# Performance work log

Measured on AMD Instinct MI355X. Metric: run time of the kernel, lower is better.

Reference implementation:

```python
import jax, jax.numpy as jnp
import numpy as np

MORA_DIV = 2


def setup_inputs() -> dict:
    key = jax.random.key(0)
    k1, k2, k3, k4 = jax.random.split(key, 4)
    d = 4096
    m = d // MORA_DIV
    x = jax.random.normal(k1, (4, 2048, d), dtype=jnp.float32)
    weight = jax.random.normal(k2, (d, d), dtype=jnp.float32) * 0.02
    mora = jax.random.normal(k3, (m, m), dtype=jnp.float32) * 0.02
    # dora_mag initialized as column L2 norm of the frozen weight (1, d_in)
    dora_mag = jnp.linalg.norm(weight, axis=0, keepdims=True)
    return {"x": x, "weight": weight, "mora": mora, "dora_mag": dora_mag}


def reference(x, weight, mora, dora_mag):
    # Tile the small adapter into full (d_out, d_in): repeat_interleave on both dims
    adapter = jnp.repeat(jnp.repeat(mora, MORA_DIV, axis=0), MORA_DIV, axis=1)
    w = weight + adapter                      # (d_out, d_in)
    col_norm = jnp.linalg.norm(w, axis=0, keepdims=True)  # (1, d_in)
    w = dora_mag * (w / col_norm)             # DoRA magnitude rescale
    return jnp.einsum('bsd,od->bso', x, w)    # F.linear, no bias
```

## Files before the change

### kernel.cpp

```cpp
#include <hip/hip_runtime.h>
#include <stdint.h>

#define M_TOT 8192
#define N_TOT 4096
#define K_TOT 4096
#define BM 256
#define BN 256
#define BK 64
#define NIT (K_TOT / (2 * BK))

typedef short  s16x8 __attribute__((ext_vector_type(8)));
typedef unsigned short u16x8 __attribute__((ext_vector_type(8)));
typedef float  f32x4 __attribute__((ext_vector_type(4)));

__device__ __forceinline__ unsigned short f32_to_bf16(float f) {
  union { float f; unsigned u; } v; v.f = f;
  unsigned r = v.u + 0x7FFFu + ((v.u >> 16) & 1u);
  return (unsigned short)(r >> 16);
}

__device__ __forceinline__ void gload_lds16(void* lds, const void* g) {
  __builtin_amdgcn_global_load_lds(
      (const __attribute__((address_space(1))) unsigned int*)g,
      (__attribute__((address_space(3))) unsigned int*)lds,
      16, 0, 0);
}

__global__ void colnorm_partial_k(const float* __restrict__ weight,
                                  const float* __restrict__ mora,
                                  float* __restrict__ partials) {
  int d = blockIdx.x * 256 + threadIdx.x;
  int o0 = blockIdx.y * 128;
  float s = 0.f;
  #pragma unroll 4
  for (int o = o0; o < o0 + 128; ++o) {
    float w = weight[(size_t)o * K_TOT + d] + mora[(size_t)(o >> 1) * 2048 + (d >> 1)];
    s = fmaf(w, w, s);
  }
  partials[blockIdx.y * K_TOT + d] = s;
}

__global__ void scale_k(const float* __restrict__ partials,
                        const float* __restrict__ dora_mag,
                        float* __restrict__ scale) {
  int d = blockIdx.x * 256 + threadIdx.x;
  float s = 0.f;
  #pragma unroll
  for (int c = 0; c < 32; ++c) s += partials[c * K_TOT + d];
  scale[d] = dora_mag[d] / sqrtf(s);
}

__global__ void pack_w_k(const float* __restrict__ weight,
                         const float* __restrict__ mora,
                         const float* __restrict__ scale,
                         unsigned short* __restrict__ wb) {
  size_t idx = ((size_t)blockIdx.x * 256 + threadIdx.x) * 8;
  int o = (int)(idx >> 12);
  int d = (int)(idx & (K_TOT - 1));
  float4 w0 = *(const float4*)(weight + idx);
  float4 w1 = *(const float4*)(weight + idx + 4);
  float4 mv = *(const float4*)(mora + (size_t)(o >> 1) * 2048 + (d >> 1));
  float4 s0 = *(const float4*)(scale + d);
  float4 s1 = *(const float4*)(scale + d + 4);
  u16x8 r;
  r[0] = f32_to_bf16((w0.x + mv.x) * s0.x);
  r[1] = f32_to_bf16((w0.y + mv.x) * s0.y);
  r[2] = f32_to_bf16((w0.z + mv.y) * s0.z);
  r[3] = f32_to_bf16((w0.w + mv.y) * s0.w);
  r[4] = f32_to_bf16((w1.x + mv.z) * s1.x);
  r[5] = f32_to_bf16((w1.y + mv.z) * s1.y);
  r[6] = f32_to_bf16((w1.z + mv.w) * s1.z);
  r[7] = f32_to_bf16((w1.w + mv.w) * s1.w);
  *(u16x8*)(wb + idx) = r;
}

__global__ void pack_x_k(const float* __restrict__ x, unsigned short* __restrict__ xb) {
  size_t idx = ((size_t)blockIdx.x * 256 + threadIdx.x) * 8;
  float4 v0 = *(const float4*)(x + idx);
  float4 v1 = *(const float4*)(x + idx + 4);
  u16x8 r;
  r[0] = f32_to_bf16(v0.x); r[1] = f32_to_bf16(v0.y);
  r[2] = f32_to_bf16(v0.z); r[3] = f32_to_bf16(v0.w);
  r[4] = f32_to_bf16(v1.x); r[5] = f32_to_bf16(v1.y);
  r[6] = f32_to_bf16(v1.z); r[7] = f32_to_bf16(v1.w);
  *(u16x8*)(xb + idx) = r;
}

__global__ void __launch_bounds__(512, 2) gemm_bf16_k(
    const unsigned short* __restrict__ xb,
    const unsigned short* __restrict__ wb,
    float* __restrict__ out) {
  __shared__ short lds[2][2][2][128 * 64];

  const int tid = threadIdx.x;
  const int l   = tid & 63;
  const int wid = tid >> 6;
  const int wm  = wid >> 2;
  const int wn  = wid & 3;
  const int wnh = wn >> 1;

  const int orig = blockIdx.x;
  const int swz  = (orig & 7) * (512 >> 3) + (orig >> 3);
  const int by = swz >> 4;
  const int bx = swz & 15;

  const unsigned short* ag = xb + (size_t)(by * BM) * K_TOT;
  const unsigned short* bg = wb + (size_t)(bx * BN) * K_TOT;

  const int row0 = tid >> 3;
  const int kb0  = (tid & 7) ^ (row0 & 7);
  const int off0 = row0 * K_TOT + kb0 * 8;
  const int off1 = off0 + 64 * K_TOT;
  const int ldst = (tid & ~63) * 8;

  const int lrow = l & 15;
  const int lq   = l >> 4;
  const int key  = lrow & 7;
  const int ab0  = lrow * 64 + ((lq) ^ key) * 8;
  const int ab1  = lrow * 64 + ((4 + lq) ^ key) * 8;

  s16x8 aA[4][2], bB[4][2];
  f32x4 acc[8][4] = {};

#define STAGE(buf, op, h, t) { \
    short* d = &lds[buf][op][h][0] + ldst; \
    const unsigned short* s = ((op) ? bg : ag) + (size_t)(h) * 128 * K_TOT + (size_t)(t) * BK; \
    gload_lds16(d, s + off0); \
    gload_lds16(d + 4096, s + off1); }
#define DSA(buf, mh) { const short* p = &lds[buf][0][wm][0]; \
    _Pragma("unroll") for (int mm = 0; mm < 4; ++mm) { \
      aA[mm][0] = *(const s16x8*)(p + ((mh) * 4 + mm) * 1024 + ab0); \
      aA[mm][1] = *(const s16x8*)(p + ((mh) * 4 + mm) * 1024 + ab1); } }
#define DSB(buf, nh) { const short* p = &lds[buf][1][wnh][0] + (wn & 1) * 4096; \
    _Pragma("unroll") for (int nn = 0; nn < 2; ++nn) { \
      bB[(nh) * 2 + nn][0] = *(const s16x8*)(p + ((nh) * 2 + nn) * 1024 + ab0); \
      bB[(nh) * 2 + nn][1] = *(const s16x8*)(p + ((nh) * 2 + nn) * 1024 + ab1); } }
#define MMQ(mh, nh) { __builtin_amdgcn_s_setprio(1); \
    _Pragma("unroll") for (int mm = 0; mm < 4; ++mm) \
      _Pragma("unroll") for (int nn = 0; nn < 2; ++nn) \
        _Pragma("unroll") for (int kh = 0; kh < 2; ++kh) \
          acc[(mh) * 4 + mm][(nh) * 2 + nn] = __builtin_amdgcn_mfma_f32_16x16x32_bf16( \
              aA[mm][kh], bB[(nh) * 2 + nn][kh], acc[(mh) * 4 + mm][(nh) * 2 + nn], 0, 0, 0); \
    __builtin_amdgcn_s_setprio(0); }
#define BARm()  asm volatile("s_barrier" ::: "memory")
#define VM6()   asm volatile("s_waitcnt vmcnt(6)" ::: "memory")
#define VM4()   asm volatile("s_waitcnt vmcnt(4)" ::: "memory")
#define VM0()   asm volatile("s_waitcnt vmcnt(0)" ::: "memory")

  STAGE(0, 0, 0, 0); STAGE(0, 0, 1, 0); STAGE(0, 1, 0, 0); STAGE(0, 1, 1, 0);
  STAGE(1, 1, 0, 1); STAGE(1, 1, 1, 1); STAGE(1, 0, 0, 1);
  VM6(); BARm();

  #pragma unroll 1
  for (int i = 0; i < NIT - 1; ++i) {
    const int t1 = 2 * i + 1;
    const int t2 = t1 + 1;
    const int t3 = t1 + 2;
    DSA(0, 0); DSB(0, 0); MMQ(0, 0); DSB(0, 1); STAGE(1, 0, 1, t1); BARm();
    MMQ(0, 1); DSA(0, 1); BARm();
    MMQ(1, 0); STAGE(0, 1, 0, t2); BARm();
    MMQ(1, 1); STAGE(0, 1, 1, t2); VM4(); BARm();
    DSA(1, 0); DSB(1, 0); MMQ(0, 0); DSB(1, 1); STAGE(0, 0, 0, t2); BARm();
    MMQ(0, 1); DSA(1, 1); STAGE(0, 0, 1, t2); BARm();
    MMQ(1, 0); STAGE(1, 1, 0, t3); BARm();
    MMQ(1, 1); STAGE(1, 1, 1, t3); STAGE(1, 0, 0, t3); VM6(); BARm();
  }

  DSA(0, 0); DSB(0, 0); MMQ(0, 0); DSB(0, 1); STAGE(1, 0, 1, 63); BARm();
  MMQ(0, 1); DSA(0, 1); BARm();
  MMQ(1, 0); BARm();
  MMQ(1, 1); VM0(); BARm();
  DSA(1, 0); DSB(1, 0); MMQ(0, 0); DSB(1, 1); BARm();
  MMQ(0, 1); DSA(1, 1); BARm();
  MMQ(1, 0); BARm();
  MMQ(1, 1);

#undef STAGE
#undef DSA
#undef DSB
#undef MMQ

  const int row0o = by * BM + wm * 128 + lq * 4;
  const int col0o = bx * BN + wn * 64 + lrow;
  #pragma unroll
  for (int m = 0; m < 8; ++m)
    #pragma unroll
    for (int n = 0; n < 4; ++n) {
      #pragma unroll
      for (int j = 0; j < 4; ++j)
        out[(size_t)(row0o + m * 16 + j) * N_TOT + col0o + n * 16] = acc[m][n][j];
    }
}

__global__ void gemm_fb_k(const float* __restrict__ x, const float* __restrict__ weight,
                          const float* __restrict__ mora, const float* __restrict__ scale,
                          float* __restrict__ out) {
  __shared__ float As[64][17];
  __shared__ float Bs[64][17];
  int t = threadIdx.x;
  int bx = blockIdx.x, by = blockIdx.y;
  int tr = t >> 4, tc = t & 15;
  float c[4][4] = {};
  for (int kt = 0; kt < K_TOT; kt += 16) {
    #pragma unroll
    for (int r = 0; r < 4; ++r) {
      int idx = r * 256 + t;
      int row = idx >> 4, col = idx & 15;
      As[row][col] = x[(size_t)(by * 64 + row) * K_TOT + kt + col];
      int o = bx * 64 + row, d = kt + col;
      Bs[row][col] = (weight[(size_t)o * K_TOT + d] + mora[(size_t)(o >> 1) * 2048 + (d >> 1)]) * scale[d];
    }
    __syncthreads();
    #pragma unroll
    for (int k = 0; k < 16; ++k) {
      float av[4], bv[4];
      #pragma unroll
      for (int i = 0; i < 4; ++i) av[i] = As[tr * 4 + i][k];
      #pragma unroll
      for (int j = 0; j < 4; ++j) bv[j] = Bs[tc * 4 + j][k];
      #pragma unroll
      for (int i = 0; i < 4; ++i)
        #pragma unroll
        for (int j = 0; j < 4; ++j)
          c[i][j] = fmaf(av[i], bv[j], c[i][j]);
    }
    __syncthreads();
  }
  #pragma unroll
  for (int i = 0; i < 4; ++i)
    #pragma unroll
    for (int j = 0; j < 4; ++j)
      out[(size_t)(by * 64 + tr * 4 + i) * N_TOT + bx * 64 + tc * 4 + j] = c[i][j];
}

extern "C" void kernel_launch(void* const* d_in, const int* in_sizes, int n_in,
                              void* d_out, int out_size, void* d_ws, size_t ws_size,
                              hipStream_t stream) {
  const float* x      = (const float*)d_in[0];
  const float* weight = (const float*)d_in[1];
  const float* mora   = (const float*)d_in[2];
  const float* dora   = (const float*)d_in[3];
  float* out = (float*)d_out;

  char* ws = (char*)d_ws;
  float* partials = (float*)ws;
  float* scale    = (float*)(ws + (512 << 10));
  const size_t OFF_W = (size_t)1 << 20;
  unsigned short* wbuf = (unsigned short*)(ws + OFF_W);
  unsigned short* xbuf = (unsigned short*)(ws + OFF_W + (size_t)N_TOT * K_TOT * 2);
  const size_t NEED = OFF_W + (size_t)N_TOT * K_TOT * 2 + (size_t)M_TOT * K_TOT * 2;

  dim3 b256(256);
  colnorm_partial_k<<<dim3(16, 32), b256, 0, stream>>>(weight, mora, partials);
  scale_k<<<16, b256, 0, stream>>>(partials, dora, scale);

  if (ws_size >= NEED) {
    pack_w_k<<<(N_TOT * K_TOT) / (256 * 8), b256, 0, stream>>>(weight, mora, scale, wbuf);
    pack_x_k<<<(M_TOT * K_TOT) / (256 * 8), b256, 0, stream>>>(x, xbuf);
    gemm_bf16_k<<<(M_TOT / BM) * (N_TOT / BN), 512, 0, stream>>>(xbuf, wbuf, out);
  } else {
    gemm_fb_k<<<dim3(N_TOT / 64, M_TOT / 64), b256, 0, stream>>>(x, weight, mora, scale, out);
  }
}
```

Baseline: 298.8 us.

## Restructure GEMM main loop to prefetch LDS fragments across phases and loosen waits

Reorders the double-buffered K loop so the LDS reads of the next half-tile's A/B fragments are issued during the preceding MFMA phase rather than at the start of the next one. Global-to-LDS stage issue is regrouped, and vmcnt waits are adjusted (8/4/2) to allow more loads in flight. The aim is to hide LDS read latency behind MFMA work and overlap global loads better. This raises the risk of LDS buffer hazards if the barrier and wait placement is wrong.

```diff
diff --git a/kernel.cpp b/kernel.cpp
--- a/kernel.cpp
+++ b/kernel.cpp
@@ -143,34 +143,37 @@
               aA[mm][kh], bB[(nh) * 2 + nn][kh], acc[(mh) * 4 + mm][(nh) * 2 + nn], 0, 0, 0); \
     __builtin_amdgcn_s_setprio(0); }
 #define BARm()  asm volatile("s_barrier" ::: "memory")
-#define VM6()   asm volatile("s_waitcnt vmcnt(6)" ::: "memory")
+#define VM8()   asm volatile("s_waitcnt vmcnt(8)" ::: "memory")
 #define VM4()   asm volatile("s_waitcnt vmcnt(4)" ::: "memory")
+#define VM2()   asm volatile("s_waitcnt vmcnt(2)" ::: "memory")
 #define VM0()   asm volatile("s_waitcnt vmcnt(0)" ::: "memory")
 
-  STAGE(0, 0, 0, 0); STAGE(0, 0, 1, 0); STAGE(0, 1, 0, 0); STAGE(0, 1, 1, 0);
-  STAGE(1, 1, 0, 1); STAGE(1, 1, 1, 1); STAGE(1, 0, 0, 1);
-  VM6(); BARm();
+  STAGE(0, 1, 0, 0); STAGE(0, 1, 1, 0); STAGE(0, 0, 0, 0); STAGE(0, 0, 1, 0);
+  STAGE(1, 1, 0, 1);
+  STAGE(1, 1, 1, 1); STAGE(1, 0, 0, 1); STAGE(1, 0, 1, 1);
+  VM8(); BARm();
+  DSA(0, 0); DSB(0, 0);
 
   #pragma unroll 1
   for (int i = 0; i < NIT - 1; ++i) {
-    const int t1 = 2 * i + 1;
-    const int t2 = t1 + 1;
-    const int t3 = t1 + 2;
-    DSA(0, 0); DSB(0, 0); MMQ(0, 0); DSB(0, 1); STAGE(1, 0, 1, t1); BARm();
+    const int t2 = 2 * i + 2;
+    const int t3 = 2 * i + 3;
+    MMQ(0, 0); DSB(0, 1); BARm();
     MMQ(0, 1); DSA(0, 1); BARm();
-    MMQ(1, 0); STAGE(0, 1, 0, t2); BARm();
-    MMQ(1, 1); STAGE(0, 1, 1, t2); VM4(); BARm();
-    DSA(1, 0); DSB(1, 0); MMQ(0, 0); DSB(1, 1); STAGE(0, 0, 0, t2); BARm();
-    MMQ(0, 1); DSA(1, 1); STAGE(0, 0, 1, t2); BARm();
-    MMQ(1, 0); STAGE(1, 1, 0, t3); BARm();
-    MMQ(1, 1); STAGE(1, 1, 1, t3); STAGE(1, 0, 0, t3); VM6(); BARm();
-  }
-
-  DSA(0, 0); DSB(0, 0); MMQ(0, 0); DSB(0, 1); STAGE(1, 0, 1, 63); BARm();
+    MMQ(1, 0); STAGE(0, 1, 0, t2); STAGE(0, 1, 1, t2); VM4(); BARm();
+    MMQ(1, 1); DSA(1, 0); DSB(1, 0); STAGE(0, 0, 0, t2); BARm();
+    MMQ(0, 0); DSB(1, 1); STAGE(0, 0, 1, t2); BARm();
+    MMQ(0, 1); DSA(1, 1); BARm();
+    MMQ(1, 0); STAGE(1, 1, 0, t3); VM2(); BARm();
+    MMQ(1, 1); DSA(0, 0); DSB(0, 0);
+    STAGE(1, 1, 1, t3); STAGE(1, 0, 0, t3); STAGE(1, 0, 1, t3); BARm();
+  }
+
+  MMQ(0, 0); DSB(0, 1); BARm();
   MMQ(0, 1); DSA(0, 1); BARm();
-  MMQ(1, 0); BARm();
-  MMQ(1, 1); VM0(); BARm();
-  DSA(1, 0); DSB(1, 0); MMQ(0, 0); DSB(1, 1); BARm();
+  MMQ(1, 0); VM0(); BARm();
+  MMQ(1, 1); DSA(1, 0); DSB(1, 0); BARm();
+  MMQ(0, 0); DSB(1, 1); BARm();
   MMQ(0, 1); DSA(1, 1); BARm();
   MMQ(1, 0); BARm();
   MMQ(1, 1);
```

Result: no change. 300.8 us (+0.7%).
